# Optimization experiments

Hardware: AMD Instinct MI355X
Metric: run time of the kernel (lower is better)

Reference implementation:

```python
import jax, jax.numpy as jnp
import numpy as np
import math

B, S, E, H = 2, 2048, 1024, 16
D = E // H  # head dim = 64


def setup_inputs() -> dict:
    key = jax.random.key(0)
    ks = jax.random.split(key, 7)
    scale = 1.0 / math.sqrt(E)
    return {
        "query": jax.random.normal(ks[0], (B, S, E), dtype=jnp.float32),
        "key": jax.random.normal(ks[1], (B, S, E), dtype=jnp.float32),
        "value": jax.random.normal(ks[2], (B, S, E), dtype=jnp.float32),
        # packed in-projection: (3E, E) weights, (3E,) bias, q/k/v order
        "in_proj_weight": jax.random.normal(ks[3], (3 * E, E), dtype=jnp.float32) * scale,
        "in_proj_bias": jnp.zeros((3 * E,), dtype=jnp.float32),
        "out_proj_weight": jax.random.normal(ks[4], (E, E), dtype=jnp.float32) * scale,
        "out_proj_bias": jnp.zeros((E,), dtype=jnp.float32),
    }


def reference(query, key, value, in_proj_weight, in_proj_bias, out_proj_weight, out_proj_bias):
    # packed in-projection (q, k, v order), F.linear convention: x @ W^T + b
    w_q, w_k, w_v = jnp.split(in_proj_weight, 3, axis=0)
    b_q, b_k, b_v = jnp.split(in_proj_bias, 3, axis=0)
    q = query @ w_q.T + b_q   # [B, S, E]
    k = key @ w_k.T + b_k
    v = value @ w_v.T + b_v

    # split heads: [B, S, E] -> [B, H, S, D]
    def heads(x):
        return x.reshape(B, S, H, D).transpose(0, 2, 1, 3)

    q, k, v = heads(q), heads(k), heads(v)
    q = q / jnp.asarray(math.sqrt(D), dtype=q.dtype)

    # naive softmax attention (materializes [B, H, S, S] as original bmm+softmax+bmm)
    scores = jnp.einsum("bhqd,bhkd->bhqk", q, k)
    attn = jax.nn.softmax(scores, axis=-1)
    out = jnp.einsum("bhqk,bhkd->bhqd", attn, v)  # [B, H, S, D]

    out = out.transpose(0, 2, 1, 3).reshape(B, S, E)
    return out @ out_proj_weight.T + out_proj_bias
```

## Files before the change

kernel.cpp:

```cpp
#include <hip/hip_runtime.h>
#include <stdint.h>

#define LOG2E 1.44269504088896340736f

typedef __bf16 bf16x8 __attribute__((ext_vector_type(8)));
typedef float f32x4 __attribute__((ext_vector_type(4)));
typedef float f32x16 __attribute__((ext_vector_type(16)));

static constexpr int Bb = 2, Ss = 2048, Ee = 1024, Hh = 16, Dd = 64;
static constexpr int BSE = Bb * Ss * Ee;

static constexpr size_t OFF_QB    = 0;
static constexpr size_t OFF_KB    = 4194304;
static constexpr size_t OFF_VB    = 8388608;
static constexpr size_t OFF_WQKV  = 12582912;
static constexpr size_t OFF_WOUT  = 15728640;
static constexpr size_t OFF_QH    = 16777216;
static constexpr size_t OFF_KH    = 20971520;
static constexpr size_t OFF_VH    = 25165824;
static constexpr size_t OFF_OB    = 29360128;

__device__ __forceinline__ uint16_t f32_bf16(float f) {
    uint32_t u = __builtin_bit_cast(uint32_t, f);
    u += 0x7fffu + ((u >> 16) & 1u);
    return (uint16_t)(u >> 16);
}

__device__ __forceinline__ uint32_t cvt_pk_bf16(float a, float b) {
    uint32_t r;
    asm("v_cvt_pk_bf16_f32 %0, %1, %2" : "=v"(r) : "v"(a), "v"(b));
    return r;
}

__device__ __forceinline__ void perm32swap(uint32_t& x, uint32_t& y) {
    asm("v_permlane32_swap_b32 %0, %1" : "+v"(x), "+v"(y));
}

__global__ __launch_bounds__(256) void cvt_kernel(
    const float* __restrict__ q, const float* __restrict__ k, const float* __restrict__ v,
    const float* __restrict__ w1, const float* __restrict__ w2, uint16_t* __restrict__ ws)
{
    const float* srcs[5] = {q, k, v, w1, w2};
    const int ns4[5] = {BSE/4, BSE/4, BSE/4, (3*Ee*Ee)/4, (Ee*Ee)/4};
    uint16_t* dsts[5] = {ws+OFF_QB, ws+OFF_KB, ws+OFF_VB, ws+OFF_WQKV, ws+OFF_WOUT};
    int z = blockIdx.z;
    int i = blockIdx.x * blockDim.x + threadIdx.x;
    if (i < ns4[z]) {
        float4 f = ((const float4*)srcs[z])[i];
        ushort4 o;
        o.x = f32_bf16(f.x); o.y = f32_bf16(f.y);
        o.z = f32_bf16(f.z); o.w = f32_bf16(f.w);
        ((ushort4*)dsts[z])[i] = o;
    }
}

template<int MODE>
__global__ __launch_bounds__(256) void gemm_nt(
    const uint16_t* __restrict__ Aq, const uint16_t* __restrict__ Ak,
    const uint16_t* __restrict__ Av, const uint16_t* __restrict__ Bw,
    const float* __restrict__ bias, uint16_t* __restrict__ OutB,
    float* __restrict__ OutF)
{
    constexpr int K = Ee, N = Ee;
    const int tid = threadIdx.x;
    const int l = tid & 63, w = tid >> 6;
    const int wr = w >> 1, wc = w & 1;
    const int z = (MODE == 0) ? blockIdx.z : 0;
    const int tm = 4 * blockIdx.x + (blockIdx.y >> 3);
    const int tn = blockIdx.y & 7;

    const uint16_t* A = (MODE == 0) ? (z == 0 ? Aq : (z == 1 ? Ak : Av)) : Aq;
    const uint16_t* Bp = Bw + (size_t)z * Ee * Ee;
    const float* bp = bias + (size_t)z * Ee;
    const size_t zoff = (size_t)(z == 2 ? 3 : z) * BSE;

    __shared__ alignas(16) uint16_t As[128 * 32];
    __shared__ alignas(16) uint16_t Bs[128 * 32];

    f32x4 acc[4][4] = {};
    const int arow = tm * 128;
    const int bcol = tn * 128;

    for (int kt = 0; kt < K / 32; ++kt) {
        __syncthreads();
        #pragma unroll
        for (int it = 0; it < 2; ++it) {
            int c = tid + it * 256;
            int row = c >> 2, qq = c & 3;
            const uint16_t* ga = A  + (size_t)(arow + row) * K + kt * 32 + qq * 8;
            const uint16_t* gb = Bp + (size_t)(bcol + row) * K + kt * 32 + qq * 8;
            __builtin_amdgcn_global_load_lds(
                (const __attribute__((address_space(1))) void*)ga,
                (__attribute__((address_space(3))) void*)(As + c * 8), 16, 0, 0);
            __builtin_amdgcn_global_load_lds(
                (const __attribute__((address_space(1))) void*)gb,
                (__attribute__((address_space(3))) void*)(Bs + c * 8), 16, 0, 0);
        }
        __syncthreads();
        bf16x8 aF[4], bF[4];
        #pragma unroll
        for (int m = 0; m < 4; ++m)
            aF[m] = *(const bf16x8*)(As + ((wr * 64 + m * 16 + (l & 15)) * 32 + (l >> 4) * 8));
        #pragma unroll
        for (int n = 0; n < 4; ++n)
            bF[n] = *(const bf16x8*)(Bs + ((wc * 64 + n * 16 + (l & 15)) * 32 + (l >> 4) * 8));
        #pragma unroll
        for (int m = 0; m < 4; ++m)
            #pragma unroll
            for (int n = 0; n < 4; ++n)
                acc[m][n] = __builtin_amdgcn_mfma_f32_16x16x32_bf16(aF[m], bF[n], acc[m][n], 0, 0, 0);
    }

    #pragma unroll
    for (int n = 0; n < 4; ++n) {
        int col = bcol + wc * 64 + n * 16 + (l & 15);
        float bn = bp[col];
        #pragma unroll
        for (int m = 0; m < 4; ++m) {
            int row0 = arow + wr * 64 + m * 16 + (l >> 4) * 4;
            #pragma unroll
            for (int j = 0; j < 4; ++j) {
                int row = row0 + j;
                float v = acc[m][n][j] + bn;
                if (MODE == 0) {
                    if (z == 0) v *= 0.125f * LOG2E;
                    int b = row >> 11, s = row & 2047, hh = col >> 6, d = col & 63;
                    OutB[zoff + (size_t)(((b * Hh) + hh) * Ss + s) * Dd + d] = f32_bf16(v);
                } else {
                    OutF[(size_t)row * N + col] = v;
                }
            }
        }
    }
}

__global__ __launch_bounds__(256) void vtr_kernel(
    const uint16_t* __restrict__ src, uint16_t* __restrict__ dst)
{
    __shared__ uint32_t T32[64][33];
    const int tid = threadIdx.x;
    const int bh = blockIdx.y;
    const int s0 = blockIdx.x * 64;
    const uint16_t* S = src + ((size_t)bh * Ss + s0) * Dd;
    {
        int rp = tid >> 3, d8 = tid & 7;
        uint4 a = *(const uint4*)(S + (size_t)(2 * rp) * Dd + d8 * 8);
        uint4 b = *(const uint4*)(S + (size_t)(2 * rp + 1) * Dd + d8 * 8);
        const uint16_t* ea = (const uint16_t*)&a;
        const uint16_t* eb = (const uint16_t*)&b;
        #pragma unroll
        for (int e = 0; e < 8; ++e)
            T32[d8 * 8 + e][rp] = (uint32_t)ea[e] | ((uint32_t)eb[e] << 16);
    }
    __syncthreads();
    uint16_t* Dp = dst + (size_t)bh * Dd * Ss + s0;
    {
        int d = tid >> 3, rpc = (tid & 7) * 4;
        #pragma unroll
        for (int half = 0; half < 2; ++half) {
            int dd = d + 32 * half;
            union { uint32_t u[4]; uint4 v; } pk;
            #pragma unroll
            for (int j = 0; j < 4; ++j) pk.u[j] = T32[dd][rpc + j];
            *(uint4*)(Dp + (size_t)dd * Ss + rpc * 2) = pk.v;
        }
    }
}

__global__ __launch_bounds__(256, 2) void attn_kernel(
    const uint16_t* __restrict__ Qh, const uint16_t* __restrict__ Kh,
    const uint16_t* __restrict__ Vtg, uint16_t* __restrict__ Ob)
{
    const int tid = threadIdx.x;
    const int l = tid & 63, w = tid >> 6;
    const int q = l & 31, hi = l >> 5;

    const int orig = blockIdx.x;
    const int L = (orig & 7) * 64 + (orig >> 3);
    const int qb = L & 15, bh = L >> 4;

    const int q0 = qb * 128;
    const size_t baseK = (size_t)bh * Ss * Dd;
    const size_t baseV = (size_t)bh * Dd * Ss;

    __shared__ alignas(16) uint16_t Ks[2][64 * 64];
    __shared__ alignas(16) uint16_t Vt[2][64 * 64];

    bf16x8 qf[4];
    {
        const uint16_t* qp = Qh + baseK + (size_t)(q0 + w * 32 + q) * Dd + hi * 8;
        #pragma unroll
        for (int m = 0; m < 4; ++m) qf[m] = *(const bf16x8*)(qp + 16 * m);
    }

    auto stage = [&](int kt, int buf) {
        const int key0 = kt * 64;
        #pragma unroll
        for (int it = 0; it < 2; ++it) {
            int c = tid + 256 * it, row = c >> 3, cc = c & 7;
            const uint16_t* gk = Kh + baseK + (size_t)(key0 + row) * Dd + ((cc ^ (row & 7)) * 8);
            __builtin_amdgcn_global_load_lds(
                (const __attribute__((address_space(1))) void*)gk,
                (__attribute__((address_space(3))) void*)(&Ks[buf][c * 8]), 16, 0, 0);
        }
        #pragma unroll
        for (int it = 0; it < 2; ++it) {
            int c = tid + 256 * it, d = c >> 3, j = c & 7;
            const uint16_t* gv = Vtg + baseV + (size_t)d * Ss + key0 + 8 * (j ^ (d & 7) ^ (d >> 3));
            __builtin_amdgcn_global_load_lds(
                (const __attribute__((address_space(1))) void*)gv,
                (__attribute__((address_space(3))) void*)(&Vt[buf][c * 8]), 16, 0, 0);
        }
    };

    stage(0, 0);

    f32x16 o0 = {}, o1 = {};
    float lsum = 0.f;

    auto build_pb = [&](const f32x16& sv, bf16x8* pbout) {
        uint32_t W[4][2];
        #pragma unroll
        for (int a = 0; a < 4; ++a) {
            float p0 = __builtin_amdgcn_exp2f(sv[4 * a + 0]);
            float p1 = __builtin_amdgcn_exp2f(sv[4 * a + 1]);
            float p2 = __builtin_amdgcn_exp2f(sv[4 * a + 2]);
            float p3 = __builtin_amdgcn_exp2f(sv[4 * a + 3]);
            lsum += (p0 + p1) + (p2 + p3);
            W[a][0] = cvt_pk_bf16(p0, p1);
            W[a][1] = cvt_pk_bf16(p2, p3);
        }
        #pragma unroll
        for (int kl = 0; kl < 2; ++kl) {
            uint32_t x0 = W[2 * kl][0], x1 = W[2 * kl][1];
            uint32_t y0 = W[2 * kl + 1][0], y1 = W[2 * kl + 1][1];
            perm32swap(x0, y0);
            perm32swap(x1, y1);
            union { uint32_t u[4]; bf16x8 v; } pu;
            pu.u[0] = x0; pu.u[1] = x1; pu.u[2] = y0; pu.u[3] = y1;
            pbout[kl] = pu.v;
        }
    };

    #pragma unroll 2
    for (int kt = 0; kt < 32; ++kt) {
        const int b = kt & 1;
        __syncthreads();

        if (kt < 31) stage(kt + 1, b ^ 1);

        f32x16 s0 = {}, s1 = {};
        __builtin_amdgcn_s_setprio(1);
        #pragma unroll
        for (int m = 0; m < 4; ++m) {
            int sw = ((2 * m + hi) ^ (q & 7)) << 3;
            bf16x8 k0 = *(const bf16x8*)&Ks[b][q * 64 + sw];
            bf16x8 k1 = *(const bf16x8*)&Ks[b][(32 + q) * 64 + sw];
            s0 = __builtin_amdgcn_mfma_f32_32x32x16_bf16(k0, qf[m], s0, 0, 0, 0);
            s1 = __builtin_amdgcn_mfma_f32_32x32x16_bf16(k1, qf[m], s1, 0, 0, 0);
        }
        __builtin_amdgcn_s_setprio(0);

        bf16x8 pb[4];
        build_pb(s0, pb + 0);
        build_pb(s1, pb + 2);

        __builtin_amdgcn_s_setprio(1);
        #pragma unroll
        for (int ka = 0; ka < 4; ++ka) {
            #pragma unroll
            for (int dt = 0; dt < 2; ++dt) {
                int d = 32 * dt + q;
                int swz = (2 * ka + hi) ^ (d & 7) ^ (d >> 3);
                bf16x8 vf = *(const bf16x8*)&Vt[b][d * 64 + swz * 8];
                if (dt == 0)
                    o0 = __builtin_amdgcn_mfma_f32_32x32x16_bf16(vf, pb[ka], o0, 0, 0, 0);
                else
                    o1 = __builtin_amdgcn_mfma_f32_32x32x16_bf16(vf, pb[ka], o1, 0, 0, 0);
            }
        }
        __builtin_amdgcn_s_setprio(0);
    }

    float lr = lsum + __shfl_xor(lsum, 32);
    const float inv = 1.0f / lr;
    __syncthreads();
    uint16_t* Os = &Ks[0][0];
    const int ql = w * 32 + q;
    #pragma unroll
    for (int dt = 0; dt < 2; ++dt) {
        const f32x16& oo = dt ? o1 : o0;
        #pragma unroll
        for (int rr = 0; rr < 16; ++rr) {
            int d = 32 * dt + (rr & 3) + 8 * (rr >> 2) + 4 * hi;
            Os[ql * 64 + (((d >> 3) ^ (ql & 7)) << 3) + (d & 7)] = f32_bf16(oo[rr] * inv);
        }
    }
    __syncthreads();
    const int bq = bh >> 4, hh = bh & 15;
    #pragma unroll
    for (int it = 0; it < 4; ++it) {
        int qr = it * 32 + (tid >> 3);
        int c = tid & 7;
        bf16x8 vv = *(const bf16x8*)&Os[qr * 64 + ((c ^ (qr & 7)) << 3)];
        *(bf16x8*)(Ob + (size_t)(bq * Ss + q0 + qr) * Ee + hh * Dd + c * 8) = vv;
    }
}

extern "C" void kernel_launch(void* const* d_in, const int* in_sizes, int n_in,
                              void* d_out, int out_size, void* d_ws, size_t ws_size,
                              hipStream_t stream) {
    (void)in_sizes; (void)n_in; (void)out_size; (void)ws_size;
    const float* query = (const float*)d_in[0];
    const float* key   = (const float*)d_in[1];
    const float* value = (const float*)d_in[2];
    const float* w_in  = (const float*)d_in[3];
    const float* b_in  = (const float*)d_in[4];
    const float* w_out = (const float*)d_in[5];
    const float* b_out = (const float*)d_in[6];
    uint16_t* ws = (uint16_t*)d_ws;

    uint16_t* qb    = ws + OFF_QB;
    uint16_t* kb    = ws + OFF_KB;
    uint16_t* vb    = ws + OFF_VB;
    uint16_t* wqkvb = ws + OFF_WQKV;
    uint16_t* woutb = ws + OFF_WOUT;
    uint16_t* Qh    = ws + OFF_QH;
    uint16_t* Kh    = ws + OFF_KH;
    uint16_t* Vtg   = ws + OFF_VH;
    uint16_t* Vsd   = ws + OFF_OB;
    uint16_t* Ob    = ws + OFF_OB;

    cvt_kernel<<<dim3(4096, 1, 5), 256, 0, stream>>>(query, key, value, w_in, w_out, ws);
    gemm_nt<0><<<dim3(8, 32, 3), 256, 0, stream>>>(qb, kb, vb, wqkvb, b_in, Qh, nullptr);
    vtr_kernel<<<dim3(32, 32), 256, 0, stream>>>(Vsd, Vtg);
    attn_kernel<<<dim3(512), 256, 0, stream>>>(Qh, Kh, Vtg, Ob);
    gemm_nt<1><<<dim3(8, 32, 1), 256, 0, stream>>>(Ob, nullptr, nullptr, woutb, b_out, nullptr, (float*)d_out);
}
```

Baseline: 127.7 us.

## Triple-buffer attention K/V staging and use smaller M tile for output GEMM

The attention kernel moves from double to triple buffering of K and V tiles in LDS. It prefetches two tiles ahead and uses an explicit vmcnt wait plus a raw barrier, so loads overlap compute further. The output projection GEMM gets a BM=64 tile variant with a 64x8 grid, doubling the block count for better CU fill. This raises LDS use in attention, which may limit occupancy, and halves per-block reuse of B in the out-projection.

```diff
diff --git a/kernel.cpp b/kernel.cpp
--- a/kernel.cpp
+++ b/kernel.cpp
@@ -54,7 +54,7 @@
     }
 }
 
-template<int MODE>
+template<int MODE, int BM>
 __global__ __launch_bounds__(256) void gemm_nt(
     const uint16_t* __restrict__ Aq, const uint16_t* __restrict__ Ak,
     const uint16_t* __restrict__ Av, const uint16_t* __restrict__ Bw,
@@ -62,50 +62,57 @@
     float* __restrict__ OutF)
 {
     constexpr int K = Ee, N = Ee;
+    constexpr int M4 = BM / 32;
     const int tid = threadIdx.x;
     const int l = tid & 63, w = tid >> 6;
     const int wr = w >> 1, wc = w & 1;
     const int z = (MODE == 0) ? blockIdx.z : 0;
-    const int tm = 4 * blockIdx.x + (blockIdx.y >> 3);
-    const int tn = blockIdx.y & 7;
+    int tm, tn;
+    if (MODE == 0) { tm = 4 * blockIdx.x + (blockIdx.y >> 3); tn = blockIdx.y & 7; }
+    else           { tm = (blockIdx.y >> 3) * 8 + blockIdx.x; tn = blockIdx.y & 7; }
 
     const uint16_t* A = (MODE == 0) ? (z == 0 ? Aq : (z == 1 ? Ak : Av)) : Aq;
     const uint16_t* Bp = Bw + (size_t)z * Ee * Ee;
     const float* bp = bias + (size_t)z * Ee;
     const size_t zoff = (size_t)(z == 2 ? 3 : z) * BSE;
 
-    __shared__ alignas(16) uint16_t As[128 * 32];
+    __shared__ alignas(16) uint16_t As[BM * 32];
     __shared__ alignas(16) uint16_t Bs[128 * 32];
 
-    f32x4 acc[4][4] = {};
-    const int arow = tm * 128;
+    f32x4 acc[M4][4] = {};
+    const int arow = tm * BM;
     const int bcol = tn * 128;
 
     for (int kt = 0; kt < K / 32; ++kt) {
         __syncthreads();
+        #pragma unroll
+        for (int it = 0; it < BM / 64; ++it) {
+            int c = tid + it * 256;
+            int row = c >> 2, qq = c & 3;
+            const uint16_t* ga = A + (size_t)(arow + row) * K + kt * 32 + qq * 8;
+            __builtin_amdgcn_global_load_lds(
+                (const __attribute__((address_space(1))) void*)ga,
+                (__attribute__((address_space(3))) void*)(As + c * 8), 16, 0, 0);
+        }
         #pragma unroll
         for (int it = 0; it < 2; ++it) {
             int c = tid + it * 256;
             int row = c >> 2, qq = c & 3;
-            const uint16_t* ga = A  + (size_t)(arow + row) * K + kt * 32 + qq * 8;
             const uint16_t* gb = Bp + (size_t)(bcol + row) * K + kt * 32 + qq * 8;
-            __builtin_amdgcn_global_load_lds(
-                (const __attribute__((address_space(1))) void*)ga,
-                (__attribute__((address_space(3))) void*)(As + c * 8), 16, 0, 0);
             __builtin_amdgcn_global_load_lds(
                 (const __attribute__((address_space(1))) void*)gb,
                 (__attribute__((address_space(3))) void*)(Bs + c * 8), 16, 0, 0);
         }
         __syncthreads();
-        bf16x8 aF[4], bF[4];
-        #pragma unroll
-        for (int m = 0; m < 4; ++m)
-            aF[m] = *(const bf16x8*)(As + ((wr * 64 + m * 16 + (l & 15)) * 32 + (l >> 4) * 8));
+        bf16x8 aF[M4], bF[4];
+        #pragma unroll
+        for (int m = 0; m < M4; ++m)
+            aF[m] = *(const bf16x8*)(As + ((wr * (BM / 2) + m * 16 + (l & 15)) * 32 + (l >> 4) * 8));
         #pragma unroll
         for (int n = 0; n < 4; ++n)
             bF[n] = *(const bf16x8*)(Bs + ((wc * 64 + n * 16 + (l & 15)) * 32 + (l >> 4) * 8));
         #pragma unroll
-        for (int m = 0; m < 4; ++m)
+        for (int m = 0; m < M4; ++m)
             #pragma unroll
             for (int n = 0; n < 4; ++n)
                 acc[m][n] = __builtin_amdgcn_mfma_f32_16x16x32_bf16(aF[m], bF[n], acc[m][n], 0, 0, 0);
@@ -116,8 +123,8 @@
         int col = bcol + wc * 64 + n * 16 + (l & 15);
         float bn = bp[col];
         #pragma unroll
-        for (int m = 0; m < 4; ++m) {
-            int row0 = arow + wr * 64 + m * 16 + (l >> 4) * 4;
+        for (int m = 0; m < M4; ++m) {
+            int row0 = arow + wr * (BM / 2) + m * 16 + (l >> 4) * 4;
             #pragma unroll
             for (int j = 0; j < 4; ++j) {
                 int row = row0 + j;
@@ -183,8 +190,8 @@
     const size_t baseK = (size_t)bh * Ss * Dd;
     const size_t baseV = (size_t)bh * Dd * Ss;
 
-    __shared__ alignas(16) uint16_t Ks[2][64 * 64];
-    __shared__ alignas(16) uint16_t Vt[2][64 * 64];
+    __shared__ alignas(16) uint16_t Ks[3][64 * 64];
+    __shared__ alignas(16) uint16_t Vt[3][64 * 64];
 
     bf16x8 qf[4];
     {
@@ -214,6 +221,7 @@
     };
 
     stage(0, 0);
+    stage(1, 1);
 
     f32x16 o0 = {}, o1 = {};
     float lsum = 0.f;
@@ -242,12 +250,13 @@
         }
     };
 
-    #pragma unroll 2
-    for (int kt = 0; kt < 32; ++kt) {
-        const int b = kt & 1;
-        __syncthreads();
-
-        if (kt < 31) stage(kt + 1, b ^ 1);
+    auto body = [&](int kt, int b, int bs, bool doIssue, bool last) {
+        if (last) asm volatile("s_waitcnt vmcnt(0)" ::: "memory");
+        else      asm volatile("s_waitcnt vmcnt(4)" ::: "memory");
+        __builtin_amdgcn_s_barrier();
+        __builtin_amdgcn_sched_barrier(0);
+
+        if (doIssue) stage(kt + 2, bs);
 
         f32x16 s0 = {}, s1 = {};
         __builtin_amdgcn_s_setprio(1);
@@ -280,7 +289,15 @@
             }
         }
         __builtin_amdgcn_s_setprio(0);
-    }
+    };
+
+    for (int u = 0; u < 30; u += 3) {
+        body(u + 0, 0, 2, true, false);
+        body(u + 1, 1, 0, true, false);
+        body(u + 2, 2, 1, true, false);
+    }
+    body(30, 0, 0, false, false);
+    body(31, 1, 0, false, true);
 
     float lr = lsum + __shfl_xor(lsum, 32);
     const float inv = 1.0f / lr;
@@ -332,8 +349,8 @@
     uint16_t* Ob    = ws + OFF_OB;
 
     cvt_kernel<<<dim3(4096, 1, 5), 256, 0, stream>>>(query, key, value, w_in, w_out, ws);
-    gemm_nt<0><<<dim3(8, 32, 3), 256, 0, stream>>>(qb, kb, vb, wqkvb, b_in, Qh, nullptr);
+    gemm_nt<0, 128><<<dim3(8, 32, 3), 256, 0, stream>>>(qb, kb, vb, wqkvb, b_in, Qh, nullptr);
     vtr_kernel<<<dim3(32, 32), 256, 0, stream>>>(Vsd, Vtg);
     attn_kernel<<<dim3(512), 256, 0, stream>>>(Qh, Kh, Vtg, Ob);
-    gemm_nt<1><<<dim3(8, 32, 1), 256, 0, stream>>>(Ob, nullptr, nullptr, woutb, b_out, nullptr, (float*)d_out);
-}
+    gemm_nt<1, 64><<<dim3(8, 64), 256, 0, stream>>>(Ob, nullptr, nullptr, woutb, b_out, nullptr, (float*)d_out);
+}
```

After: 123.8 us. 3.1% less time.
